# Optimization experiments

Measured on AMD Instinct MI355X. Metric: run time of the kernel, lower is better.

## Reference

```python
import jax, jax.numpy as jnp
import numpy as np

N, IN_DIM, OUT_DIM, HEADS = 8192, 256, 64, 2

def setup_inputs() -> dict:
    key = jax.random.key(0)
    k1, k2, k3, k4, k5 = jax.random.split(key, 5)
    x = jax.random.normal(k1, (N, IN_DIM), dtype=jnp.float32)
    adj = jax.random.randint(k2, (N, N), 0, 2, dtype=jnp.int32)
    # nn.Linear(in_dim, out_dim*heads, bias=False): weight [out_dim*heads, in_dim]
    W = jax.random.normal(k3, (OUT_DIM * HEADS, IN_DIM), dtype=jnp.float32) / np.sqrt(IN_DIM)
    attn_l = jax.random.normal(k4, (HEADS, OUT_DIM), dtype=jnp.float32)
    attn_r = jax.random.normal(k5, (HEADS, OUT_DIM), dtype=jnp.float32)
    return {"x": x, "adj": adj, "W": W, "attn_l": attn_l, "attn_r": attn_r}

def reference(x, adj, W, attn_l, attn_r):
    n = x.shape[0]
    h = (x @ W.T).reshape(n, HEADS, OUT_DIM)          # [N, H, D]
    el = jnp.einsum('nhd,hd->nh', h, attn_l)           # [N, H]
    er = jnp.einsum('nhd,hd->nh', h, attn_r)           # [N, H]
    e = el[:, None, :] + er[None, :, :]                # [N, N, H]
    e = jnp.where(adj[:, :, None] == 0, -jnp.inf, e)
    a = jax.nn.softmax(e, axis=1)                      # softmax over source nodes j
    out = jnp.einsum('ijh,jhd->ihd', a, h)             # [N, H, D]
    return out.reshape(n, HEADS * OUT_DIM)
```

## Files before the change

### kernel.cpp

```cpp
#include <hip/hip_runtime.h>
#include <cstdint>
#include <cstddef>

#define N_NODES 8192
#define IN_DIM  256
#define OUT_DIM 64
#define HEADS   2
#define FEAT    128
#define NTILES  9
#define ACC_STRIDE 132
#define KSPLIT  8

typedef __bf16 bf16x8 __attribute__((ext_vector_type(8)));
typedef float  f32x4  __attribute__((ext_vector_type(4)));
typedef int    i32x4  __attribute__((ext_vector_type(4)));
typedef unsigned uu32x4 __attribute__((ext_vector_type(4)));

static __device__ __forceinline__ unsigned short f2bf(float f) {
  unsigned u = __float_as_uint(f);
  u += 0x7FFFu + ((u >> 16) & 1u);
  return (unsigned short)(u >> 16);
}

__global__ void k_vr(const float* __restrict__ W, const float* __restrict__ attn_r,
                     float* __restrict__ vr) {
  const int t = threadIdx.x;
  const int h = t >> 8, k = t & 255;
  float s = 0.f;
  for (int d = 0; d < OUT_DIM; d++)
    s += attn_r[h*OUT_DIM + d] * W[(size_t)(h*OUT_DIM + d)*IN_DIM + k];
  vr[h*IN_DIM + k] = s;
}

__global__ __launch_bounds__(256) void k_h(const float* __restrict__ x,
                                           const float* __restrict__ W,
                                           float* __restrict__ H) {
  const int rb = blockIdx.x >> 1, cb = blockIdx.x & 1;
  __shared__ float xs[64][68];
  __shared__ float wl[64][68];
  const int tid = threadIdx.x;
  const int ty = tid >> 4, tx = tid & 15;
  float acc[4][4] = {};
  for (int kc = 0; kc < IN_DIM; kc += 64) {
    __syncthreads();
#pragma unroll
    for (int p = 0; p < 4; p++) {
      const int idx = p*256 + tid;
      const int r = idx >> 4, k4 = idx & 15;
      *(float4*)&xs[r][k4*4] = *(const float4*)(x + (size_t)(rb*64 + r)*IN_DIM + kc + k4*4);
      *(float4*)&wl[r][k4*4] = *(const float4*)(W + (size_t)(cb*64 + r)*IN_DIM + kc + k4*4);
    }
    __syncthreads();
#pragma unroll
    for (int k4 = 0; k4 < 16; k4++) {
      float4 xr[4], wr[4];
#pragma unroll
      for (int i = 0; i < 4; i++) {
        xr[i] = *(const float4*)&xs[ty + i*16][k4*4];
        wr[i] = *(const float4*)&wl[tx + i*16][k4*4];
      }
#pragma unroll
      for (int i = 0; i < 4; i++)
#pragma unroll
        for (int j = 0; j < 4; j++)
          acc[i][j] += xr[i].x*wr[j].x + xr[i].y*wr[j].y + xr[i].z*wr[j].z + xr[i].w*wr[j].w;
    }
  }
#pragma unroll
  for (int i = 0; i < 4; i++)
#pragma unroll
    for (int j = 0; j < 4; j++)
      H[(size_t)(rb*64 + ty + i*16)*FEAT + cb*64 + tx + j*16] = acc[i][j];
}

__global__ void k_er(const float* __restrict__ x, const float* __restrict__ vr,
                     float* __restrict__ er) {
  const int wave = threadIdx.x >> 6, lane = threadIdx.x & 63;
  const int j = blockIdx.x*4 + wave;
  float4 xv = ((const float4*)(x + (size_t)j*IN_DIM))[lane];
  float4 a0 = ((const float4*)vr)[lane];
  float4 a1 = ((const float4*)(vr + IN_DIM))[lane];
  float s0 = xv.x*a0.x + xv.y*a0.y + xv.z*a0.z + xv.w*a0.w;
  float s1 = xv.x*a1.x + xv.y*a1.y + xv.z*a1.z + xv.w*a1.w;
#pragma unroll
  for (int off = 32; off > 0; off >>= 1) {
    s0 += __shfl_down(s0, off);
    s1 += __shfl_down(s1, off);
  }
  if (lane == 0) { er[j*2+0] = s0; er[j*2+1] = s1; }
}

__global__ void k_pack(const float* __restrict__ H, const float* __restrict__ er,
                       unsigned short* __restrict__ frag) {
  const int oct = blockIdx.x;
  const int c = threadIdx.x;
  if (c >= 144) return;
  const int j0 = oct * 8;
  const int kb = oct >> 2, sub = oct & 3;
  unsigned short v[8];
  if (c < FEAT) {
    const int h = c >> 6;
#pragma unroll
    for (int t = 0; t < 8; t++) {
      float w = __expf(er[(j0 + t)*2 + h]);
      v[t] = f2bf(w * H[(size_t)(j0 + t)*FEAT + c]);
    }
  } else if (c < FEAT + HEADS) {
    const int h = c - FEAT;
#pragma unroll
    for (int t = 0; t < 8; t++) v[t] = f2bf(__expf(er[(j0 + t)*2 + h]));
  } else {
#pragma unroll
    for (int t = 0; t < 8; t++) v[t] = 0;
  }
  uint4 o;
  o.x = (unsigned)v[0] | ((unsigned)v[1] << 16);
  o.y = (unsigned)v[2] | ((unsigned)v[3] << 16);
  o.z = (unsigned)v[4] | ((unsigned)v[5] << 16);
  o.w = (unsigned)v[6] | ((unsigned)v[7] << 16);
  uint4* dst = (uint4*)frag + ((size_t)(kb*NTILES + (c >> 4)))*64 + (sub*16 + (c & 15));
  *dst = o;
}

__global__ __launch_bounds__(256, 2) void k_main(const int* __restrict__ adj,
                                                 const uint4* __restrict__ fragB,
                                                 float* __restrict__ accum) {
  const int mb = blockIdx.x >> 3;
  const int ks = blockIdx.x & 7;
  const int tid = threadIdx.x;
  const int wave = tid >> 6, lane = tid & 63;
  const int m16 = lane & 15, quad = lane >> 4;

  const int row0 = mb*128 + wave*32 + m16;
  const int* a0 = adj + (size_t)row0*N_NODES + ks*1024 + quad*8;
  const int* a1 = a0 + (size_t)16*N_NODES;
  const uint4* bb = fragB + (size_t)(ks*32)*NTILES*64 + lane;

  f32x4 acc0[NTILES], acc1[NTILES];
#pragma unroll
  for (int n = 0; n < NTILES; n++) {
    acc0[n] = (f32x4){0.f, 0.f, 0.f, 0.f};
    acc1[n] = (f32x4){0.f, 0.f, 0.f, 0.f};
  }

  i32x4  Abuf[2][4];
  uu32x4 Bbuf[2][NTILES];

  auto loadA = [&](int kk, int buf) {
    const i32x4* p0 = (const i32x4*)(a0 + kk*32);
    const i32x4* p1 = (const i32x4*)(a1 + kk*32);
    Abuf[buf][0] = __builtin_nontemporal_load(p0);
    Abuf[buf][1] = __builtin_nontemporal_load(p0 + 1);
    Abuf[buf][2] = __builtin_nontemporal_load(p1);
    Abuf[buf][3] = __builtin_nontemporal_load(p1 + 1);
  };
  auto loadB = [&](int kk, int buf) {
    const uu32x4* b = (const uu32x4*)bb;
#pragma unroll
    for (int t = 0; t < NTILES; t++)
      Bbuf[buf][t] = b[(size_t)(kk*NTILES + t)*64];
  };
  auto conv = [&](const i32x4* A) -> bf16x8 {
    const int* ai = (const int*)A;
    unsigned u0 = (ai[0] ? 0x3F80u : 0u) | (ai[1] ? 0x3F800000u : 0u);
    unsigned u1 = (ai[2] ? 0x3F80u : 0u) | (ai[3] ? 0x3F800000u : 0u);
    unsigned u2 = (ai[4] ? 0x3F80u : 0u) | (ai[5] ? 0x3F800000u : 0u);
    unsigned u3 = (ai[6] ? 0x3F80u : 0u) | (ai[7] ? 0x3F800000u : 0u);
    uu32x4 u = {u0, u1, u2, u3};
    return __builtin_bit_cast(bf16x8, u);
  };
  auto compute = [&](int buf) {
    bf16x8 af0 = conv(&Abuf[buf][0]);
    bf16x8 af1 = conv(&Abuf[buf][2]);
#pragma unroll
    for (int n = 0; n < NTILES; n++) {
      bf16x8 bfr = __builtin_bit_cast(bf16x8, Bbuf[buf][n]);
      acc0[n] = __builtin_amdgcn_mfma_f32_16x16x32_bf16(af0, bfr, acc0[n], 0, 0, 0);
    }
#pragma unroll
    for (int n = 0; n < NTILES; n++) {
      bf16x8 bfr = __builtin_bit_cast(bf16x8, Bbuf[buf][n]);
      acc1[n] = __builtin_amdgcn_mfma_f32_16x16x32_bf16(af1, bfr, acc1[n], 0, 0, 0);
    }
  };

  loadA(0, 0); loadB(0, 0);
  for (int kk = 0; kk < 32; kk += 2) {
    loadA(kk + 1, 1); loadB(kk + 1, 1);
    compute(0);
    const int k2 = (kk + 2 < 32) ? kk + 2 : 31;
    loadA(k2, 0); loadB(k2, 0);
    compute(1);
  }

  const int rb0 = mb*128 + wave*32 + quad*4;
  float* op = accum + (size_t)ks*N_NODES*ACC_STRIDE;
#pragma unroll
  for (int n = 0; n < NTILES; n++) {
    if (n == 8 && m16 >= HEADS) continue;
#pragma unroll
    for (int r = 0; r < 4; r++) {
      op[(size_t)(rb0 + r)*ACC_STRIDE + n*16 + m16]      = acc0[n][r];
      op[(size_t)(rb0 + 16 + r)*ACC_STRIDE + n*16 + m16] = acc1[n][r];
    }
  }
}

__global__ void k_div(const float* __restrict__ acc, float* __restrict__ out) {
  const int i = blockIdx.x, c = threadIdx.x;
  const int h = c >> 6;
  float num = 0.f, den = 0.f;
#pragma unroll
  for (int s = 0; s < KSPLIT; s++) {
    const float* p = acc + ((size_t)s*N_NODES + i)*ACC_STRIDE;
    num += p[c];
    den += p[FEAT + h];
  }
  out[(size_t)i*FEAT + c] = num / den;
}

extern "C" void kernel_launch(void* const* d_in, const int* in_sizes, int n_in,
                              void* d_out, int out_size, void* d_ws, size_t ws_size,
                              hipStream_t stream) {
  const float* x      = (const float*)d_in[0];
  const int*   adj    = (const int*)  d_in[1];
  const float* W      = (const float*)d_in[2];
  const float* attn_r = (const float*)d_in[4];

  char* ws = (char*)d_ws;
  float* vr            = (float*)(ws + 0);
  float* er            = (float*)(ws + 4096);
  float* H             = (float*)(ws + 131072);
  unsigned short* frag = (unsigned short*)(ws + 4325376);
  float* acc           = (float*)(ws + 6684672);
  float* out           = (float*)d_out;

  hipLaunchKernelGGL(k_vr,   dim3(1),    dim3(512), 0, stream, W, attn_r, vr);
  hipLaunchKernelGGL(k_h,    dim3(256),  dim3(256), 0, stream, x, W, H);
  hipLaunchKernelGGL(k_er,   dim3(2048), dim3(256), 0, stream, x, vr, er);
  hipLaunchKernelGGL(k_pack, dim3(1024), dim3(192), 0, stream, H, er, frag);
  hipLaunchKernelGGL(k_main, dim3(512),  dim3(256), 0, stream, adj, (const uint4*)frag, acc);
  hipLaunchKernelGGL(k_div,  dim3(8192), dim3(128), 0, stream, acc, out);
}
```

Before: 440.8 us.

## Pre-pack adjacency into bitmask and feed main MFMA kernel from bits

Adds a separate pass that reads the int32 adjacency matrix once at full bandwidth and packs each row into a bitmask laid out to match the MFMA A-fragment order. The main kernel then loads only a few words per lane up front and expands bits to bf16 ones/zeros in registers, so it no longer streams 256 MB of adjacency inside its MFMA loop. The full adjacency read still happens, now in its own launch, and the bitmask costs an extra workspace write and read, so the gain depends on the standalone pass streaming better than the interleaved loads did.

```diff
diff --git a/kernel.cpp b/kernel.cpp
--- a/kernel.cpp
+++ b/kernel.cpp
@@ -122,8 +122,29 @@
   *dst = o;
 }
 
-__global__ __launch_bounds__(256, 2) void k_main(const int* __restrict__ adj,
-                                                 const uint4* __restrict__ fragB,
+__global__ __launch_bounds__(1024) void k_bits(const int* __restrict__ adj,
+                                               unsigned* __restrict__ bits) {
+  const int row = blockIdx.x, tid = threadIdx.x;
+  const int* p = adj + (size_t)row*N_NODES + tid*8;
+  i32x4 a = *(const i32x4*)p;
+  i32x4 b = *(const i32x4*)(p + 4);
+  unsigned byte =
+      (unsigned)(a.x != 0)       | ((unsigned)(a.y != 0) << 1) |
+      ((unsigned)(a.z != 0) << 2) | ((unsigned)(a.w != 0) << 3) |
+      ((unsigned)(b.x != 0) << 4) | ((unsigned)(b.y != 0) << 5) |
+      ((unsigned)(b.z != 0) << 6) | ((unsigned)(b.w != 0) << 7);
+  unsigned b1 = __shfl_down(byte, 4);
+  unsigned b2 = __shfl_down(byte, 8);
+  unsigned b3 = __shfl_down(byte, 12);
+  if (((tid >> 2) & 3) == 0) {
+    unsigned w = byte | (b1 << 8) | (b2 << 16) | (b3 << 24);
+    const int ks = tid >> 7, g = (tid >> 4) & 7, quad = tid & 3;
+    bits[(size_t)row*256 + ks*32 + g*4 + quad] = w;
+  }
+}
+
+__global__ __launch_bounds__(256, 2) void k_main(const unsigned* __restrict__ bits,
+                                                 const uu32x4* __restrict__ fragB,
                                                  float* __restrict__ accum) {
   const int mb = blockIdx.x >> 3;
   const int ks = blockIdx.x & 7;
@@ -132,9 +153,15 @@
   const int m16 = lane & 15, quad = lane >> 4;
 
   const int row0 = mb*128 + wave*32 + m16;
-  const int* a0 = adj + (size_t)row0*N_NODES + ks*1024 + quad*8;
-  const int* a1 = a0 + (size_t)16*N_NODES;
-  const uint4* bb = fragB + (size_t)(ks*32)*NTILES*64 + lane;
+  const uu32x4* bb = fragB + (size_t)(ks*32)*NTILES*64 + lane;
+
+  unsigned wA[8], wB[8];
+  {
+    const unsigned* pa = bits + (size_t)row0*256 + ks*32 + quad;
+    const unsigned* pb = pa + 16*256;
+#pragma unroll
+    for (int g = 0; g < 8; g++) { wA[g] = pa[g*4]; wB[g] = pb[g*4]; }
+  }
 
   f32x4 acc0[NTILES], acc1[NTILES];
 #pragma unroll
@@ -143,35 +170,24 @@
     acc1[n] = (f32x4){0.f, 0.f, 0.f, 0.f};
   }
 
-  i32x4  Abuf[2][4];
   uu32x4 Bbuf[2][NTILES];
-
-  auto loadA = [&](int kk, int buf) {
-    const i32x4* p0 = (const i32x4*)(a0 + kk*32);
-    const i32x4* p1 = (const i32x4*)(a1 + kk*32);
-    Abuf[buf][0] = __builtin_nontemporal_load(p0);
-    Abuf[buf][1] = __builtin_nontemporal_load(p0 + 1);
-    Abuf[buf][2] = __builtin_nontemporal_load(p1);
-    Abuf[buf][3] = __builtin_nontemporal_load(p1 + 1);
+  auto loadB = [&](int kk, int buf) {
+#pragma unroll
+    for (int t = 0; t < NTILES; t++)
+      Bbuf[buf][t] = bb[(size_t)(kk*NTILES + t)*64];
   };
-  auto loadB = [&](int kk, int buf) {
-    const uu32x4* b = (const uu32x4*)bb;
-#pragma unroll
-    for (int t = 0; t < NTILES; t++)
-      Bbuf[buf][t] = b[(size_t)(kk*NTILES + t)*64];
-  };
-  auto conv = [&](const i32x4* A) -> bf16x8 {
-    const int* ai = (const int*)A;
-    unsigned u0 = (ai[0] ? 0x3F80u : 0u) | (ai[1] ? 0x3F800000u : 0u);
-    unsigned u1 = (ai[2] ? 0x3F80u : 0u) | (ai[3] ? 0x3F800000u : 0u);
-    unsigned u2 = (ai[4] ? 0x3F80u : 0u) | (ai[5] ? 0x3F800000u : 0u);
-    unsigned u3 = (ai[6] ? 0x3F80u : 0u) | (ai[7] ? 0x3F800000u : 0u);
+  auto expand = [&](unsigned m) -> bf16x8 {
+    unsigned u0 = ((m & 1u)   ? 0x3F80u : 0u) | ((m & 2u)   ? 0x3F800000u : 0u);
+    unsigned u1 = ((m & 4u)   ? 0x3F80u : 0u) | ((m & 8u)   ? 0x3F800000u : 0u);
+    unsigned u2 = ((m & 16u)  ? 0x3F80u : 0u) | ((m & 32u)  ? 0x3F800000u : 0u);
+    unsigned u3 = ((m & 64u)  ? 0x3F80u : 0u) | ((m & 128u) ? 0x3F800000u : 0u);
     uu32x4 u = {u0, u1, u2, u3};
     return __builtin_bit_cast(bf16x8, u);
   };
-  auto compute = [&](int buf) {
-    bf16x8 af0 = conv(&Abuf[buf][0]);
-    bf16x8 af1 = conv(&Abuf[buf][2]);
+  auto compute = [&](int kk, int buf) {
+    const int g = kk >> 2, t = kk & 3;
+    bf16x8 af0 = expand((wA[g] >> (t*8)) & 0xffu);
+    bf16x8 af1 = expand((wB[g] >> (t*8)) & 0xffu);
 #pragma unroll
     for (int n = 0; n < NTILES; n++) {
       bf16x8 bfr = __builtin_bit_cast(bf16x8, Bbuf[buf][n]);
@@ -184,13 +200,12 @@
     }
   };
 
-  loadA(0, 0); loadB(0, 0);
+  loadB(0, 0);
   for (int kk = 0; kk < 32; kk += 2) {
-    loadA(kk + 1, 1); loadB(kk + 1, 1);
-    compute(0);
-    const int k2 = (kk + 2 < 32) ? kk + 2 : 31;
-    loadA(k2, 0); loadB(k2, 0);
-    compute(1);
+    loadB(kk + 1, 1);
+    compute(kk, 0);
+    loadB((kk + 2 < 32) ? kk + 2 : 31, 0);
+    compute(kk + 1, 1);
   }
 
   const int rb0 = mb*128 + wave*32 + quad*4;
@@ -232,13 +247,16 @@
   float* er            = (float*)(ws + 4096);
   float* H             = (float*)(ws + 131072);
   unsigned short* frag = (unsigned short*)(ws + 4325376);
-  float* acc           = (float*)(ws + 6684672);
+  unsigned* bits       = (unsigned*)(ws + 6684672);
+  float* acc           = (float*)(ws + 15073280);
   float* out           = (float*)d_out;
 
   hipLaunchKernelGGL(k_vr,   dim3(1),    dim3(512), 0, stream, W, attn_r, vr);
   hipLaunchKernelGGL(k_h,    dim3(256),  dim3(256), 0, stream, x, W, H);
   hipLaunchKernelGGL(k_er,   dim3(2048), dim3(256), 0, stream, x, vr, er);
   hipLaunchKernelGGL(k_pack, dim3(1024), dim3(192), 0, stream, H, er, frag);
-  hipLaunchKernelGGL(k_main, dim3(512),  dim3(256), 0, stream, adj, (const uint4*)frag, acc);
+  hipLaunchKernelGGL(k_bits, dim3(8192), dim3(1024), 0, stream, adj, bits);
+  hipLaunchKernelGGL(k_main, dim3(512),  dim3(256), 0, stream, bits,
+                     (const uu32x4*)frag, acc);
   hipLaunchKernelGGL(k_div,  dim3(8192), dim3(128), 0, stream, acc, out);
 }
```

Result: slower. 466.7 us (+5.9%).

## Fuse projection, er scoring, exp weighting and fragment packing into one prep kernel

Applied to the files above, without the earlier changes.

Replaces four preprocessing kernels (vr, H GEMM, er, pack) with a single k_prep kernel. Each block computes 32 rows of H over all 128 features, derives er directly from H by shuffle reduction with attn_r, applies exp weights, and writes bf16 MFMA fragments through shared memory. This removes three launches and the global round trips of H and er. In exchange each block reloads the full W tile, and the block count for the prep stage drops to 256.

```diff
diff --git a/kernel.cpp b/kernel.cpp
--- a/kernel.cpp
+++ b/kernel.cpp
@@ -22,104 +22,100 @@
   return (unsigned short)(u >> 16);
 }
 
-__global__ void k_vr(const float* __restrict__ W, const float* __restrict__ attn_r,
-                     float* __restrict__ vr) {
-  const int t = threadIdx.x;
-  const int h = t >> 8, k = t & 255;
-  float s = 0.f;
-  for (int d = 0; d < OUT_DIM; d++)
-    s += attn_r[h*OUT_DIM + d] * W[(size_t)(h*OUT_DIM + d)*IN_DIM + k];
-  vr[h*IN_DIM + k] = s;
-}
-
-__global__ __launch_bounds__(256) void k_h(const float* __restrict__ x,
-                                           const float* __restrict__ W,
-                                           float* __restrict__ H) {
-  const int rb = blockIdx.x >> 1, cb = blockIdx.x & 1;
-  __shared__ float xs[64][68];
-  __shared__ float wl[64][68];
+__global__ __launch_bounds__(256) void k_prep(const float* __restrict__ x,
+                                              const float* __restrict__ W,
+                                              const float* __restrict__ attn_r,
+                                              uint4* __restrict__ frag) {
+  const int kb = blockIdx.x;
   const int tid = threadIdx.x;
-  const int ty = tid >> 4, tx = tid & 15;
-  float acc[4][4] = {};
+  const int tx = tid & 15, ty = tid >> 4;
+  const int j0 = kb * 32;
+
+  __shared__ float xs[32][68];
+  __shared__ float wl[128][68];
+  __shared__ unsigned short pk[32][146];
+
+  float acc[2][8] = {};
+
   for (int kc = 0; kc < IN_DIM; kc += 64) {
     __syncthreads();
 #pragma unroll
-    for (int p = 0; p < 4; p++) {
-      const int idx = p*256 + tid;
-      const int r = idx >> 4, k4 = idx & 15;
-      *(float4*)&xs[r][k4*4] = *(const float4*)(x + (size_t)(rb*64 + r)*IN_DIM + kc + k4*4);
-      *(float4*)&wl[r][k4*4] = *(const float4*)(W + (size_t)(cb*64 + r)*IN_DIM + kc + k4*4);
+    for (int p = 0; p < 2; p++) {
+      const int slot = p*256 + tid;
+      const int r = slot >> 4, k4 = slot & 15;
+      *(float4*)&xs[r][k4*4] = *(const float4*)(x + (size_t)(j0 + r)*IN_DIM + kc + k4*4);
+    }
+#pragma unroll
+    for (int p = 0; p < 8; p++) {
+      const int slot = p*256 + tid;
+      const int r = slot >> 4, k4 = slot & 15;
+      *(float4*)&wl[r][k4*4] = *(const float4*)(W + (size_t)r*IN_DIM + kc + k4*4);
     }
     __syncthreads();
 #pragma unroll
     for (int k4 = 0; k4 < 16; k4++) {
-      float4 xr[4], wr[4];
-#pragma unroll
-      for (int i = 0; i < 4; i++) {
-        xr[i] = *(const float4*)&xs[ty + i*16][k4*4];
-        wr[i] = *(const float4*)&wl[tx + i*16][k4*4];
-      }
-#pragma unroll
-      for (int i = 0; i < 4; i++)
-#pragma unroll
-        for (int j = 0; j < 4; j++)
-          acc[i][j] += xr[i].x*wr[j].x + xr[i].y*wr[j].y + xr[i].z*wr[j].z + xr[i].w*wr[j].w;
-    }
-  }
-#pragma unroll
-  for (int i = 0; i < 4; i++)
-#pragma unroll
-    for (int j = 0; j < 4; j++)
-      H[(size_t)(rb*64 + ty + i*16)*FEAT + cb*64 + tx + j*16] = acc[i][j];
-}
-
-__global__ void k_er(const float* __restrict__ x, const float* __restrict__ vr,
-                     float* __restrict__ er) {
-  const int wave = threadIdx.x >> 6, lane = threadIdx.x & 63;
-  const int j = blockIdx.x*4 + wave;
-  float4 xv = ((const float4*)(x + (size_t)j*IN_DIM))[lane];
-  float4 a0 = ((const float4*)vr)[lane];
-  float4 a1 = ((const float4*)(vr + IN_DIM))[lane];
-  float s0 = xv.x*a0.x + xv.y*a0.y + xv.z*a0.z + xv.w*a0.w;
-  float s1 = xv.x*a1.x + xv.y*a1.y + xv.z*a1.z + xv.w*a1.w;
-#pragma unroll
-  for (int off = 32; off > 0; off >>= 1) {
-    s0 += __shfl_down(s0, off);
-    s1 += __shfl_down(s1, off);
-  }
-  if (lane == 0) { er[j*2+0] = s0; er[j*2+1] = s1; }
-}
-
-__global__ void k_pack(const float* __restrict__ H, const float* __restrict__ er,
-                       unsigned short* __restrict__ frag) {
-  const int oct = blockIdx.x;
-  const int c = threadIdx.x;
-  if (c >= 144) return;
-  const int j0 = oct * 8;
-  const int kb = oct >> 2, sub = oct & 3;
-  unsigned short v[8];
-  if (c < FEAT) {
-    const int h = c >> 6;
-#pragma unroll
-    for (int t = 0; t < 8; t++) {
-      float w = __expf(er[(j0 + t)*2 + h]);
-      v[t] = f2bf(w * H[(size_t)(j0 + t)*FEAT + c]);
-    }
-  } else if (c < FEAT + HEADS) {
-    const int h = c - FEAT;
-#pragma unroll
-    for (int t = 0; t < 8; t++) v[t] = f2bf(__expf(er[(j0 + t)*2 + h]));
-  } else {
-#pragma unroll
-    for (int t = 0; t < 8; t++) v[t] = 0;
-  }
-  uint4 o;
-  o.x = (unsigned)v[0] | ((unsigned)v[1] << 16);
-  o.y = (unsigned)v[2] | ((unsigned)v[3] << 16);
-  o.z = (unsigned)v[4] | ((unsigned)v[5] << 16);
-  o.w = (unsigned)v[6] | ((unsigned)v[7] << 16);
-  uint4* dst = (uint4*)frag + ((size_t)(kb*NTILES + (c >> 4)))*64 + (sub*16 + (c & 15));
-  *dst = o;
+      float4 xr[2], wr[8];
+#pragma unroll
+      for (int i = 0; i < 2; i++) xr[i] = *(const float4*)&xs[ty + i*16][k4*4];
+#pragma unroll
+      for (int jj = 0; jj < 8; jj++) wr[jj] = *(const float4*)&wl[tx + jj*16][k4*4];
+#pragma unroll
+      for (int i = 0; i < 2; i++)
+#pragma unroll
+        for (int jj = 0; jj < 8; jj++)
+          acc[i][jj] += xr[i].x*wr[jj].x + xr[i].y*wr[jj].y +
+                        xr[i].z*wr[jj].z + xr[i].w*wr[jj].w;
+    }
+  }
+
+  float ar[8];
+#pragma unroll
+  for (int jj = 0; jj < 8; jj++)
+    ar[jj] = attn_r[((jj >> 2)) * OUT_DIM + ((tx + jj*16) & 63)];
+  float e0[2] = {}, e1[2] = {};
+#pragma unroll
+  for (int i = 0; i < 2; i++) {
+#pragma unroll
+    for (int jj = 0; jj < 4; jj++) e0[i] += acc[i][jj] * ar[jj];
+#pragma unroll
+    for (int jj = 4; jj < 8; jj++) e1[i] += acc[i][jj] * ar[jj];
+  }
+#pragma unroll
+  for (int m = 1; m <= 8; m <<= 1) {
+#pragma unroll
+    for (int i = 0; i < 2; i++) {
+      e0[i] += __shfl_xor(e0[i], m);
+      e1[i] += __shfl_xor(e1[i], m);
+    }
+  }
+  float w0[2], w1[2];
+#pragma unroll
+  for (int i = 0; i < 2; i++) { w0[i] = __expf(e0[i]); w1[i] = __expf(e1[i]); }
+
+#pragma unroll
+  for (int i = 0; i < 2; i++) {
+    const int row = ty + i*16;
+#pragma unroll
+    for (int jj = 0; jj < 8; jj++)
+      pk[row][tx + jj*16] = f2bf((jj < 4 ? w0[i] : w1[i]) * acc[i][jj]);
+    pk[row][128 + tx] = (tx == 0) ? f2bf(w0[i]) : (tx == 1) ? f2bf(w1[i]) : 0;
+  }
+  __syncthreads();
+
+#pragma unroll
+  for (int t = 0; t < 3; t++) {
+    const int wid = t*256 + tid;
+    if (wid < 576) {
+      const int l = wid & 63, n = wid >> 6;
+      const int col = n*16 + (l & 15), jb = (l >> 4) * 8;
+      uint4 o;
+      o.x = (unsigned)pk[jb+0][col] | ((unsigned)pk[jb+1][col] << 16);
+      o.y = (unsigned)pk[jb+2][col] | ((unsigned)pk[jb+3][col] << 16);
+      o.z = (unsigned)pk[jb+4][col] | ((unsigned)pk[jb+5][col] << 16);
+      o.w = (unsigned)pk[jb+6][col] | ((unsigned)pk[jb+7][col] << 16);
+      frag[((size_t)kb*NTILES + n)*64 + l] = o;
+    }
+  }
 }
 
 __global__ __launch_bounds__(256, 2) void k_main(const int* __restrict__ adj,
@@ -228,17 +224,11 @@
   const float* attn_r = (const float*)d_in[4];
 
   char* ws = (char*)d_ws;
-  float* vr            = (float*)(ws + 0);
-  float* er            = (float*)(ws + 4096);
-  float* H             = (float*)(ws + 131072);
-  unsigned short* frag = (unsigned short*)(ws + 4325376);
-  float* acc           = (float*)(ws + 6684672);
-  float* out           = (float*)d_out;
-
-  hipLaunchKernelGGL(k_vr,   dim3(1),    dim3(512), 0, stream, W, attn_r, vr);
-  hipLaunchKernelGGL(k_h,    dim3(256),  dim3(256), 0, stream, x, W, H);
-  hipLaunchKernelGGL(k_er,   dim3(2048), dim3(256), 0, stream, x, vr, er);
-  hipLaunchKernelGGL(k_pack, dim3(1024), dim3(192), 0, stream, H, er, frag);
-  hipLaunchKernelGGL(k_main, dim3(512),  dim3(256), 0, stream, adj, (const uint4*)frag, acc);
+  uint4* frag = (uint4*)(ws + 0);
+  float* acc  = (float*)(ws + 4194304);
+  float* out  = (float*)d_out;
+
+  hipLaunchKernelGGL(k_prep, dim3(256),  dim3(256), 0, stream, x, W, attn_r, frag);
+  hipLaunchKernelGGL(k_main, dim3(512),  dim3(256), 0, stream, adj, frag, acc);
   hipLaunchKernelGGL(k_div,  dim3(8192), dim3(128), 0, stream, acc, out);
 }
```

Result: faster. 432.0 us (-2.0%).
